# Performance work log

Measured on AMD Instinct MI355X. Metric: run time of the kernel, lower is better.

Reference implementation:

```python
import jax, jax.numpy as jnp
import numpy as np

DIM = 2048
N_HEADS = 32
N_KV_HEADS = 8
HEAD_DIM = 64
REPEATS = N_HEADS // N_KV_HEADS
SCALE = HEAD_DIM ** -0.5
L = 2048
B = 1


def rotary_matrix(context_len, d):
    # Dense (L, d, d) RoPE rotation matrix, exactly as get_rotary_matrix1.
    pos = jnp.arange(1, context_len + 1, dtype=jnp.float32)[:, None]
    i = jnp.arange(d // 2)
    theta = 10000.0 ** (-2.0 * i.astype(jnp.float32) / d)
    m_theta = pos * theta  # (L, d/2)
    cos_v, sin_v = jnp.cos(m_theta), jnp.sin(m_theta)
    R = jnp.zeros((context_len, d, d), dtype=jnp.float32)
    R = R.at[:, 2 * i, 2 * i].set(cos_v)
    R = R.at[:, 2 * i, 2 * i + 1].set(-sin_v)
    R = R.at[:, 2 * i + 1, 2 * i].set(sin_v)
    R = R.at[:, 2 * i + 1, 2 * i + 1].set(cos_v)
    return R


def causal_mask(context_len):
    idx = jnp.arange(context_len)
    return (idx[:, None] < idx[None, :]).astype(jnp.float32) * -1e9


def setup_inputs() -> dict:
    key = jax.random.key(0)
    ks = jax.random.split(key, 5)
    x = jax.random.normal(ks[0], (B, L, DIM), dtype=jnp.float32)
    mask = causal_mask(L)
    wq_w = jax.random.normal(ks[1], (N_HEADS * HEAD_DIM, DIM), dtype=jnp.float32) * 0.02
    wk_w = jax.random.normal(ks[2], (N_KV_HEADS * HEAD_DIM, DIM), dtype=jnp.float32) * 0.02
    wv_w = jax.random.normal(ks[3], (N_KV_HEADS * HEAD_DIM, DIM), dtype=jnp.float32) * 0.02
    wo_w = jax.random.normal(ks[4], (DIM, N_HEADS * HEAD_DIM), dtype=jnp.float32) * 0.02
    return {"x": x, "mask": mask, "wq_w": wq_w, "wk_w": wk_w, "wv_w": wv_w, "wo_w": wo_w}


def reference(x, mask, wq_w, wk_w, wv_w, wo_w):
    Bx, Lx, D = x.shape
    # projections (torch Linear: y = x @ W.T)
    q = jnp.einsum('bld,od->blo', x, wq_w).reshape(Bx, Lx, N_HEADS, HEAD_DIM).transpose(0, 2, 1, 3)
    k = jnp.einsum('bld,od->blo', x, wk_w).reshape(Bx, Lx, N_KV_HEADS, HEAD_DIM).transpose(0, 2, 1, 3)
    v = jnp.einsum('bld,od->blo', x, wv_w).reshape(Bx, Lx, N_KV_HEADS, HEAD_DIM).transpose(0, 2, 1, 3)
    # GQA repeat of kv heads (interleaved, matching concat-unsqueeze-reshape)
    k = jnp.repeat(k, REPEATS, axis=1)
    v = jnp.repeat(v, REPEATS, axis=1)
    # dense-matrix RoPE on q and (repeated) k
    R = rotary_matrix(Lx, HEAD_DIM)
    q = jnp.einsum('bhlj,lij->bhli', q, R)
    k = jnp.einsum('bhlj,lij->bhli', k, R)
    scores = jnp.einsum('bhld,bhmd->bhlm', q, k) * SCALE + mask
    attn = jax.nn.softmax(scores.astype(jnp.float32), axis=-1)
    out = jnp.einsum('bhlm,bhmd->bhld', attn, v)
    out = out.transpose(0, 2, 1, 3).reshape(Bx, Lx, N_HEADS * HEAD_DIM)
    out = jnp.einsum('blo,do->bld', out, wo_w)
    return out, k, v
```

## Files before the change

### kernel.cpp

```cpp
#include <hip/hip_runtime.h>

typedef __bf16 bf16;
typedef __bf16 bf16x8 __attribute__((ext_vector_type(8)));
typedef float floatx4 __attribute__((ext_vector_type(4)));
typedef float floatx16 __attribute__((ext_vector_type(16)));
typedef unsigned int uint;

#define MFMA16(a, b, c) __builtin_amdgcn_mfma_f32_16x16x32_bf16((a), (b), (c), 0, 0, 0)
#define MFMA32(a, b, c) __builtin_amdgcn_mfma_f32_32x32x16_bf16((a), (b), (c), 0, 0, 0)

__device__ __forceinline__ void gl2lds16(const bf16* g, bf16* l) {
  __builtin_amdgcn_global_load_lds(
      (const __attribute__((address_space(1))) void*)g,
      (__attribute__((address_space(3))) void*)l, 16, 0, 0);
}
__device__ __forceinline__ void wait_vm0() { __builtin_amdgcn_s_waitcnt(0x0f70); }

__device__ __forceinline__ float* slot_ptr(int s, float* o0, float* o1) {
  return s < 512 ? o0 + (size_t)s * 8192 : o1 + (size_t)(s - 512) * 8192;
}
__device__ __forceinline__ const float* slot_ptr_c(int s, const float* o0,
                                                   const float* o1) {
  return s < 512 ? o0 + (size_t)s * 8192 : o1 + (size_t)(s - 512) * 8192;
}

__device__ __forceinline__ void cvt8(const float* __restrict__ s,
                                     bf16* __restrict__ d, int i8) {
  const float4 a = ((const float4*)s)[i8 * 2];
  const float4 b = ((const float4*)s)[i8 * 2 + 1];
  bf16x8 o;
  o[0] = (bf16)a.x; o[1] = (bf16)a.y; o[2] = (bf16)a.z; o[3] = (bf16)a.w;
  o[4] = (bf16)b.x; o[5] = (bf16)b.y; o[6] = (bf16)b.z; o[7] = (bf16)b.w;
  *(bf16x8*)(d + i8 * 8) = o;
}

__global__ __launch_bounds__(256) void convert_kernel(
    const float* __restrict__ x, const float* __restrict__ wq,
    const float* __restrict__ wk, const float* __restrict__ wv,
    const float* __restrict__ wo, bf16* __restrict__ xb,
    bf16* __restrict__ wqb, bf16* __restrict__ wkb, bf16* __restrict__ wvb,
    bf16* __restrict__ wob) {
  const int g = blockIdx.x * 256 + threadIdx.x;
  if (g < 524288) cvt8(x, xb, g);
  else if (g < 1048576) cvt8(wq, wqb, g - 524288);
  else if (g < 1179648) cvt8(wk, wkb, g - 1048576);
  else if (g < 1310720) cvt8(wv, wvb, g - 1179648);
  else cvt8(wo, wob, g - 1310720);
}

template <typename OutT>
__device__ __forceinline__ void gemm_tile_body64(
    const bf16* __restrict__ A, int lda,
    const bf16* __restrict__ B, int ldb,
    OutT* __restrict__ C, int ldc, int K,
    bf16* S) {
  const int t = threadIdx.x;
  const int w = t >> 6, lane = t & 63;
  const int l15 = lane & 15, qd = lane >> 4;
  const int wr = w >> 1, wc = w & 1;

  floatx4 acc[2][4];
#pragma unroll
  for (int i = 0; i < 2; ++i)
#pragma unroll
    for (int j = 0; j < 4; ++j) acc[i][j] = (floatx4){0.f, 0.f, 0.f, 0.f};

  const bf16* gb[6];
  int lo[6];
#pragma unroll
  for (int i = 0; i < 6; ++i) {
    const int u = w + 4 * i;
    lo[i] = u * 512 + lane * 8;
    if (u < 8) {
      gb[i] = A + ((u >> 1) * 16 + l15) * lda + (u & 1) * 32 + qd * 8;
    } else {
      const int v = u - 8;
      gb[i] = B + ((v >> 1) * 16 + l15) * ldb + (v & 1) * 32 + qd * 8;
    }
  }

#define STG64(kt_, buf_)                                            \
  {                                                                 \
    bf16* d_ = S + (buf_) * 12288;                                  \
    _Pragma("unroll")                                               \
    for (int i_ = 0; i_ < 6; ++i_)                                  \
      gl2lds16(gb[i_] + (kt_) * 64, d_ + lo[i_]);                   \
  }

  const int NT = K >> 6;
  STG64(0, 0);
  wait_vm0();
  __syncthreads();
  int cur = 0;
  for (int kt = 0; kt < NT; ++kt) {
    if (kt + 1 < NT) STG64(kt + 1, cur ^ 1);
    const bf16* Ab = S + cur * 12288;
    const bf16* Bb = Ab + 4096;
    bf16x8 a[2][2], b[4][2];
#pragma unroll
    for (int i = 0; i < 2; ++i)
#pragma unroll
      for (int kk = 0; kk < 2; ++kk)
        a[i][kk] =
            *(const bf16x8*)(Ab + ((wr * 2 + i) * 2 + kk) * 512 + lane * 8);
#pragma unroll
    for (int j = 0; j < 4; ++j)
#pragma unroll
      for (int kk = 0; kk < 2; ++kk)
        b[j][kk] =
            *(const bf16x8*)(Bb + ((wc * 4 + j) * 2 + kk) * 512 + lane * 8);
#pragma unroll
    for (int kk = 0; kk < 2; ++kk)
#pragma unroll
      for (int i = 0; i < 2; ++i)
#pragma unroll
        for (int j = 0; j < 4; ++j)
          acc[i][j] = MFMA16(a[i][kk], b[j][kk], acc[i][j]);
    wait_vm0();
    __builtin_amdgcn_sched_barrier(0);
    __builtin_amdgcn_s_barrier();
    __builtin_amdgcn_sched_barrier(0);
    cur ^= 1;
  }
#undef STG64

#pragma unroll
  for (int i = 0; i < 2; ++i)
#pragma unroll
    for (int j = 0; j < 4; ++j) {
      const int row = wr * 32 + i * 16 + qd * 4;
      const int col = wc * 64 + j * 16 + l15;
#pragma unroll
      for (int r = 0; r < 4; ++r)
        C[(row + r) * ldc + col] = (OutT)acc[i][j][r];
    }
}

__global__ __launch_bounds__(256) void gemm_qkv(
    const bf16* __restrict__ x, const bf16* __restrict__ wq,
    const bf16* __restrict__ wk, const bf16* __restrict__ wv,
    bf16* __restrict__ Qws, bf16* __restrict__ Kh, bf16* __restrict__ Vh,
    bf16* __restrict__ Vt) {
  __shared__ bf16 SM[17152];
  bf16* As = SM;
  bf16* Bs = SM + 4096;
  const int bid = blockIdx.y * 24 + blockIdx.x;
  const int swz = (bid & 7) * 48 + (bid >> 3);
  const int nb = swz % 24;
  const int m0 = (swz / 24) * 128;
  const bf16* B;
  if (nb < 16) B = wq + nb * 128 * 2048;
  else if (nb < 20) B = wk + (nb - 16) * 128 * 2048;
  else B = wv + (nb - 20) * 128 * 2048;

  const int t = threadIdx.x;
  const int w = t >> 6, lane = t & 63;
  const int l15 = lane & 15, qd = lane >> 4;
  const int wr = w >> 1, wc = w & 1;

  floatx4 acc[4][4];
#pragma unroll
  for (int i = 0; i < 4; ++i)
#pragma unroll
    for (int j = 0; j < 4; ++j) acc[i][j] = (floatx4){0.f, 0.f, 0.f, 0.f};

  const bf16* A = x + m0 * 2048;
  const int mt0 = w, mt1 = w + 4;
  const int kseg = qd * 8;
  const bf16* ga0 = A + (mt0 * 16 + l15) * 2048 + kseg;
  const bf16* ga1 = A + (mt1 * 16 + l15) * 2048 + kseg;
  const bf16* gb0 = B + (mt0 * 16 + l15) * 2048 + kseg;
  const bf16* gb1 = B + (mt1 * 16 + l15) * 2048 + kseg;
  bf16* lA0 = As + mt0 * 512 + lane * 8;
  bf16* lA1 = As + mt1 * 512 + lane * 8;
  bf16* lB0 = Bs + mt0 * 512 + lane * 8;
  bf16* lB1 = Bs + mt1 * 512 + lane * 8;

  for (int k0 = 0; k0 < 2048; k0 += 32) {
    gl2lds16(ga0 + k0, lA0);
    gl2lds16(ga1 + k0, lA1);
    gl2lds16(gb0 + k0, lB0);
    gl2lds16(gb1 + k0, lB1);
    wait_vm0();
    __syncthreads();

    bf16x8 a[4], b[4];
#pragma unroll
    for (int i = 0; i < 4; ++i)
      a[i] = *(const bf16x8*)(As + (wr * 4 + i) * 512 + lane * 8);
#pragma unroll
    for (int j = 0; j < 4; ++j)
      b[j] = *(const bf16x8*)(Bs + (wc * 4 + j) * 512 + lane * 8);
#pragma unroll
    for (int i = 0; i < 4; ++i)
#pragma unroll
      for (int j = 0; j < 4; ++j) acc[i][j] = MFMA16(a[i], b[j], acc[i][j]);
    __syncthreads();
  }

#pragma unroll
  for (int i = 0; i < 4; ++i)
#pragma unroll
    for (int j = 0; j < 4; ++j) {
      const int row = wr * 64 + i * 16 + qd * 4;
      const int col = wc * 64 + j * 16 + l15;
#pragma unroll
      for (int r = 0; r < 4; ++r)
        SM[(row + r) * 134 + col] = (bf16)acc[i][j][r];
    }
  __syncthreads();

  const float NEG_LOG2_10000_D32 = -0.4152410118609203f;
  if (nb < 16) {
#pragma unroll
    for (int k = 0; k < 8; ++k) {
      const int u = t + (k << 8);
      const int row = u >> 4, c8 = (u & 15) << 3;
      const bf16x8 v = *(const bf16x8*)&SM[row * 134 + c8];
      const float base = (float)(m0 + row + 1);
      bf16x8 ov;
#pragma unroll
      for (int p = 0; p < 4; ++p) {
        const int a = ((c8 & 63) >> 1) + p;
        float s, c;
        __sincosf(base * exp2f(NEG_LOG2_10000_D32 * (float)a), &s, &c);
        const float x0 = (float)v[2 * p], x1 = (float)v[2 * p + 1];
        ov[2 * p] = (bf16)(c * x0 - s * x1);
        ov[2 * p + 1] = (bf16)(s * x0 + c * x1);
      }
      *(bf16x8*)&Qws[(m0 + row) * 2048 + nb * 128 + c8] = ov;
    }
  } else if (nb < 20) {
#pragma unroll
    for (int k = 0; k < 8; ++k) {
      const int u = t + (k << 8);
      const int row = u >> 4, c8 = (u & 15) << 3;
      const bf16x8 v = *(const bf16x8*)&SM[row * 134 + c8];
      const float base = (float)(m0 + row + 1);
      bf16x8 ov;
#pragma unroll
      for (int p = 0; p < 4; ++p) {
        const int a = ((c8 & 63) >> 1) + p;
        float s, c;
        __sincosf(base * exp2f(NEG_LOG2_10000_D32 * (float)a), &s, &c);
        const float x0 = (float)v[2 * p], x1 = (float)v[2 * p + 1];
        ov[2 * p] = (bf16)(c * x0 - s * x1);
        ov[2 * p + 1] = (bf16)(s * x0 + c * x1);
      }
      const int g512 = (nb - 16) * 128 + c8;
      const int kvh = g512 >> 6, d8 = g512 & 63;
      *(bf16x8*)&Kh[(kvh * 2048 + m0 + row) * 64 + d8] = ov;
    }
  } else {
#pragma unroll
    for (int k = 0; k < 8; ++k) {
      const int u = t + (k << 8);
      const int row = u >> 4, c8 = (u & 15) << 3;
      const bf16x8 v = *(const bf16x8*)&SM[row * 134 + c8];
      const int g512 = (nb - 20) * 128 + c8;
      const int kvh = g512 >> 6, d8 = g512 & 63;
      *(bf16x8*)&Vh[(kvh * 2048 + m0 + row) * 64 + d8] = v;
    }
#pragma unroll
    for (int k = 0; k < 8; ++k) {
      const int u = t + (k << 8);
      const int col = u >> 4, r8 = (u & 15) << 3;
      bf16x8 v;
#pragma unroll
      for (int jj = 0; jj < 8; ++jj) v[jj] = SM[(r8 + jj) * 134 + col];
      const int g512 = (nb - 20) * 128 + col;
      const int kvh = g512 >> 6, d = g512 & 63;
      *(bf16x8*)&Vt[kvh * 131072 + d * 2048 + m0 + r8] = v;
    }
  }
}

__global__ __launch_bounds__(256) void gemm_o(
    const bf16* __restrict__ Ows, const bf16* __restrict__ wo,
    float* __restrict__ out, const bf16* __restrict__ Kh,
    const bf16* __restrict__ Vh, float* __restrict__ kout,
    float* __restrict__ vout) {
  __shared__ bf16 S[24576];
  const int bid = blockIdx.y * 16 + blockIdx.x;
  const int swz = (bid & 7) * 64 + (bid >> 3);
  const int n0 = (swz & 15) * 128;
  const int m0 = (swz >> 4) * 64;
  gemm_tile_body64<float>(Ows + m0 * 2048, 2048, wo + n0 * 2048, 2048,
                          out + m0 * 2048 + n0, 2048, 2048, S);

  const int g = bid * 256 + (int)threadIdx.x;
  for (uint u = (uint)g; u < 262144u; u += 131072u) {
    const uint u2 = u & 131071u;
    const bf16* src = (u < 131072u) ? Kh : Vh;
    float* dst = (u < 131072u) ? kout : vout;
    const int kvh2 = u2 >> 14;
    const int rr = u2 & 16383;
    const int l = rr >> 3, d8 = (rr & 7) * 8;
    const bf16x8 v = *(const bf16x8*)(src + (kvh2 * 2048 + l) * 64 + d8);
    float4 f0, f1;
    f0.x = (float)v[0]; f0.y = (float)v[1]; f0.z = (float)v[2]; f0.w = (float)v[3];
    f1.x = (float)v[4]; f1.y = (float)v[5]; f1.z = (float)v[6]; f1.w = (float)v[7];
#pragma unroll
    for (int rep = 0; rep < 4; ++rep) {
      float* o2 = dst + (((kvh2 * 4 + rep) * 2048 + l) * 64 + d8);
      *(float4*)o2 = f0;
      *(float4*)(o2 + 4) = f1;
    }
  }
}

__global__ __launch_bounds__(256) void flash_kernel(
    const bf16* __restrict__ Qws, const bf16* __restrict__ Kh,
    const bf16* __restrict__ Vt, bf16* __restrict__ Ows,
    float* __restrict__ Op0, float* __restrict__ Op1, float* __restrict__ ML) {
  __shared__ bf16 SMEM[16384];

  const int h = blockIdx.y;
  const int bx = blockIdx.x;
  int qt, seg, kts, kte, slot;
  if (bx < 4) {
    qt = bx; seg = -1; kts = 0; kte = 2 * qt + 2; slot = -1;
  } else if (bx < 12) {
    const int j = bx - 4;
    qt = 4 + (j >> 1); seg = j & 1;
    const int nkt = 2 * qt + 2;
    kts = seg * nkt / 2; kte = (seg + 1) * nkt / 2;
    slot = h * 32 + (bx - 4);
  } else {
    const int j = bx - 12;
    qt = 8 + j / 3; seg = j % 3;
    const int nkt = 2 * qt + 2;
    kts = seg * nkt / 3; kte = (seg + 1) * nkt / 3;
    slot = h * 32 + (bx - 4);
  }
  const int kh = h >> 2;
  const int q0 = qt * 128;
  const int t = threadIdx.x, w = t >> 6, lane = t & 63;
  const int l31 = lane & 31, hf = lane >> 5;
  const int qw = q0 + w * 32;

  const int s0 = w, s1 = w + 4;
  const bf16* gK0 = Kh + kh * 131072 + ((s0 >> 2) * 32 + l31) * 64 + (s0 & 3) * 16 + hf * 8;
  const bf16* gK1 = Kh + kh * 131072 + ((s1 >> 2) * 32 + l31) * 64 + (s1 & 3) * 16 + hf * 8;
  const bf16* gV0 = Vt + kh * 131072 + ((s0 >> 2) * 32 + l31) * 2048 + (s0 & 3) * 16 + hf * 8;
  const bf16* gV1 = Vt + kh * 131072 + ((s1 >> 2) * 32 + l31) * 2048 + (s1 & 3) * 16 + hf * 8;

  {
    const int nb = kts & 1;
    gl2lds16(gK0 + kts * 4096, &SMEM[nb * 8192 + s0 * 512 + lane * 8]);
    gl2lds16(gK1 + kts * 4096, &SMEM[nb * 8192 + s1 * 512 + lane * 8]);
    gl2lds16(gV0 + kts * 64, &SMEM[nb * 8192 + 4096 + s0 * 512 + lane * 8]);
    gl2lds16(gV1 + kts * 64, &SMEM[nb * 8192 + 4096 + s1 * 512 + lane * 8]);
  }

  bf16x8 qf[4];
  {
    const bf16* qrow = Qws + (qw + l31) * 2048 + h * 64 + hf * 8;
#pragma unroll
    for (int c = 0; c < 4; ++c) qf[c] = *(const bf16x8*)(qrow + c * 16);
  }

  floatx16 o[2] = {};
  float mrun = -3e38f, lrun = 0.f;

  const float C = 0.1803368801f;
  for (int kt = kts; kt < kte; ++kt) {
    wait_vm0();
    __syncthreads();
    if (kt + 1 < kte) {
      const int nb = (kt + 1) & 1;
      const int koff = (kt + 1) * 4096, voff = (kt + 1) * 64;
      gl2lds16(gK0 + koff, &SMEM[nb * 8192 + s0 * 512 + lane * 8]);
      gl2lds16(gK1 + koff, &SMEM[nb * 8192 + s1 * 512 + lane * 8]);
      gl2lds16(gV0 + voff, &SMEM[nb * 8192 + 4096 + s0 * 512 + lane * 8]);
      gl2lds16(gV1 + voff, &SMEM[nb * 8192 + 4096 + s1 * 512 + lane * 8]);
    }
    const int kt64 = kt * 64;
    if (kt64 > qw + 31) continue;
    const bf16* Kb = &SMEM[(kt & 1) * 8192];
    const bf16* Vb = Kb + 4096;

    floatx16 st[2];
    __builtin_amdgcn_s_setprio(1);
#pragma unroll
    for (int tt = 0; tt < 2; ++tt) {
      floatx16 z = {};
#pragma unroll
      for (int c = 0; c < 4; ++c) {
        const bf16x8 kf = *(const bf16x8*)(Kb + (tt * 4 + c) * 512 + lane * 8);
        z = MFMA32(kf, qf[c], z);
      }
      st[tt] = z;
    }
    __builtin_amdgcn_s_setprio(0);
    if (kt64 + 64 > qw) {
      const int myq = qw + l31;
#pragma unroll
      for (int tt = 0; tt < 2; ++tt)
#pragma unroll
        for (int r = 0; r < 16; ++r) {
          const int key = kt64 + tt * 32 + (r & 3) + 8 * (r >> 2) + 4 * hf;
          if (key > myq) st[tt][r] = -1e30f;
        }
    }
    float ma = -3e38f, mb = -3e38f, mc = -3e38f, md = -3e38f;
#pragma unroll
    for (int tt = 0; tt < 2; ++tt)
#pragma unroll
      for (int r = 0; r < 16; r += 4) {
        ma = fmaxf(ma, st[tt][r + 0]);
        mb = fmaxf(mb, st[tt][r + 1]);
        mc = fmaxf(mc, st[tt][r + 2]);
        md = fmaxf(md, st[tt][r + 3]);
      }
    float mx = fmaxf(fmaxf(ma, mb), fmaxf(mc, md));
    mx = fmaxf(mx, __shfl_xor(mx, 32));
    const bool defer = __all((mx - mrun) * C <= 8.f);
    if (!defer) {
      const float mn = fmaxf(mrun, mx);
      const float al = __builtin_amdgcn_exp2f((mrun - mn) * C);
      lrun *= al;
#pragma unroll
      for (int n = 0; n < 2; ++n)
#pragma unroll
        for (int r = 0; r < 16; ++r) o[n][r] *= al;
      mrun = mn;
    }
    float ra = 0.f, rb = 0.f, rc = 0.f, rd = 0.f;
#pragma unroll
    for (int tt = 0; tt < 2; ++tt)
#pragma unroll
      for (int r = 0; r < 16; r += 4) {
        const float p0 = __builtin_amdgcn_exp2f((st[tt][r + 0] - mrun) * C);
        const float p1 = __builtin_amdgcn_exp2f((st[tt][r + 1] - mrun) * C);
        const float p2 = __builtin_amdgcn_exp2f((st[tt][r + 2] - mrun) * C);
        const float p3 = __builtin_amdgcn_exp2f((st[tt][r + 3] - mrun) * C);
        st[tt][r + 0] = p0; ra += p0;
        st[tt][r + 1] = p1; rb += p1;
        st[tt][r + 2] = p2; rc += p2;
        st[tt][r + 3] = p3; rd += p3;
      }
    float rs = (ra + rb) + (rc + rd);
    rs += __shfl_xor(rs, 32);
    lrun += rs;

    uint pk[2][4][2];
#pragma unroll
    for (int tt = 0; tt < 2; ++tt)
#pragma unroll
      for (int g = 0; g < 4; ++g)
#pragma unroll
        for (int p = 0; p < 2; ++p) {
          union { bf16 h2[2]; uint u; } cv;
          cv.h2[0] = (bf16)st[tt][4 * g + 2 * p];
          cv.h2[1] = (bf16)st[tt][4 * g + 2 * p + 1];
          pk[tt][g][p] = cv.u;
        }
    uint own_[2][2][2], rv[2][2][2];
#pragma unroll
    for (int tt = 0; tt < 2; ++tt)
#pragma unroll
      for (int gam = 0; gam < 2; ++gam)
#pragma unroll
        for (int p = 0; p < 2; ++p) {
          own_[tt][gam][p] = hf ? pk[tt][2 * gam + 1][p] : pk[tt][2 * gam][p];
          const uint snd = hf ? pk[tt][2 * gam][p] : pk[tt][2 * gam + 1][p];
          rv[tt][gam][p] = (uint)__shfl_xor((int)snd, 32);
        }
    __builtin_amdgcn_s_setprio(1);
#pragma unroll
    for (int c = 0; c < 4; ++c) {
      const int tt = c >> 1, gam = c & 1;
      union { uint u[4]; bf16x8 v; } pf;
      pf.u[0] = hf ? rv[tt][gam][0] : own_[tt][gam][0];
      pf.u[1] = hf ? rv[tt][gam][1] : own_[tt][gam][1];
      pf.u[2] = hf ? own_[tt][gam][0] : rv[tt][gam][0];
      pf.u[3] = hf ? own_[tt][gam][1] : rv[tt][gam][1];
#pragma unroll
      for (int n = 0; n < 2; ++n)
        o[n] = MFMA32(*(const bf16x8*)(Vb + (n * 4 + c) * 512 + lane * 8),
                      pf.v, o[n]);
    }
    __builtin_amdgcn_s_setprio(0);
  }

  if (seg < 0) {
    __syncthreads();
    bf16* Osh = SMEM;
    const float inv = 1.f / lrun;
#pragma unroll
    for (int n = 0; n < 2; ++n)
#pragma unroll
      for (int r = 0; r < 16; ++r) {
        const int dl = n * 32 + (r & 3) + 8 * (r >> 2) + 4 * hf;
        Osh[(w * 32 + l31) * 66 + dl] = (bf16)(o[n][r] * inv);
      }
    __syncthreads();
#pragma unroll
    for (int i = 0; i < 4; ++i) {
      const int row = (t >> 3) + i * 32;
      const int col = (t & 7) * 8;
      const bf16x8 vv = *(const bf16x8*)&Osh[row * 66 + col];
      *(bf16x8*)&Ows[(q0 + row) * 2048 + h * 64 + col] = vv;
    }
  } else {
    float* Op = slot_ptr(slot, Op0, Op1);
#pragma unroll
    for (int n = 0; n < 2; ++n)
#pragma unroll
      for (int r = 0; r < 16; ++r) {
        const int dl = n * 32 + (r & 3) + 8 * (r >> 2) + 4 * hf;
        Op[dl * 128 + w * 32 + l31] = o[n][r];
      }
    if (hf == 0) {
      ML[slot * 256 + w * 32 + l31] = mrun;
      ML[slot * 256 + 128 + w * 32 + l31] = lrun;
    }
  }
}

__global__ __launch_bounds__(256) void combine_kernel(
    const float* __restrict__ Op0, const float* __restrict__ Op1,
    const float* __restrict__ ML, bf16* __restrict__ Ows) {
  __shared__ bf16 Osh[128 * 66];
  const int b = blockIdx.x;
  const int h = b / 12, qi = b % 12;
  const int qt = 4 + qi;
  const int q0 = qt * 128;
  const bool three = (qi >= 4);
  const int slot0 = h * 32 + (three ? 8 + (qi - 4) * 3 : qi * 2);
  const int t = threadIdx.x;
  const int row = t & 127, dh = t >> 7;
  const float C = 0.1803368801f;
  const float m0 = ML[(slot0 + 0) * 256 + row], l0 = ML[(slot0 + 0) * 256 + 128 + row];
  const float m1 = ML[(slot0 + 1) * 256 + row], l1 = ML[(slot0 + 1) * 256 + 128 + row];
  const float m2 = three ? ML[(slot0 + 2) * 256 + row] : -3e38f;
  const float l2 = three ? ML[(slot0 + 2) * 256 + 128 + row] : 0.f;
  const float m = fmaxf(fmaxf(m0, m1), m2);
  const float w0 = __builtin_amdgcn_exp2f((m0 - m) * C);
  const float w1 = __builtin_amdgcn_exp2f((m1 - m) * C);
  const float w2 = three ? __builtin_amdgcn_exp2f((m2 - m) * C) : 0.f;
  const float inv = 1.f / (l0 * w0 + l1 * w1 + l2 * w2);
  const float* P0 = slot_ptr_c(slot0 + 0, Op0, Op1);
  const float* P1 = slot_ptr_c(slot0 + 1, Op0, Op1);
  const float* P2 = three ? slot_ptr_c(slot0 + 2, Op0, Op1) : P0;
#pragma unroll
  for (int j = 0; j < 32; ++j) {
    const int d = dh * 32 + j;
    const float v = (P0[d * 128 + row] * w0 + P1[d * 128 + row] * w1 +
                     P2[d * 128 + row] * w2) *
                    inv;
    Osh[row * 66 + d] = (bf16)v;
  }
  __syncthreads();
#pragma unroll
  for (int i = 0; i < 4; ++i) {
    const int r2 = (t >> 3) + i * 32;
    const int col = (t & 7) * 8;
    const bf16x8 vv = *(const bf16x8*)&Osh[r2 * 66 + col];
    *(bf16x8*)&Ows[(q0 + r2) * 2048 + h * 64 + col] = vv;
  }
}

extern "C" void kernel_launch(void* const* d_in, const int* in_sizes, int n_in,
                              void* d_out, int out_size, void* d_ws,
                              size_t ws_size, hipStream_t stream) {
  const float* x = (const float*)d_in[0];
  const float* wq = (const float*)d_in[2];
  const float* wk = (const float*)d_in[3];
  const float* wv = (const float*)d_in[4];
  const float* wo = (const float*)d_in[5];

  float* out = (float*)d_out;
  float* kout = out + 4194304;
  float* vout = out + 8388608;

  bf16* ws = (bf16*)d_ws;
  bf16* xb = ws;
  bf16* wqb = xb + 4194304;
  bf16* wkb = wqb + 4194304;
  bf16* wvb = wkb + 1048576;
  bf16* wob = wvb + 1048576;
  bf16* Qws = wob + 4194304;
  bf16* Kws = Qws + 4194304;
  bf16* Vh = Kws + 1048576;
  bf16* Vt = Vh + 1048576;
  bf16* Ows = Vt + 1048576;
  bf16* Kh = Ows + 4194304;
  float* Op0 = out;
  float* Op1 = (float*)ws;
  float* MLf = (float*)Kws;

  convert_kernel<<<dim3(7168), dim3(256), 0, stream>>>(x, wq, wk, wv, wo, xb,
                                                       wqb, wkb, wvb, wob);
  gemm_qkv<<<dim3(24, 16), dim3(256), 0, stream>>>(xb, wqb, wkb, wvb, Qws, Kh,
                                                   Vh, Vt);
  flash_kernel<<<dim3(36, 32), dim3(256), 0, stream>>>(Qws, Kh, Vt, Ows, Op0,
                                                       Op1, MLf);
  combine_kernel<<<dim3(384), dim3(256), 0, stream>>>(Op0, Op1, MLf, Ows);
  gemm_o<<<dim3(16, 32), dim3(256), 0, stream>>>(Ows, wob, out, Kh, Vh, kout,
                                                 vout);
}
```

Baseline: 282.1 us.

## Deepen QKV GEMM K-step, reverse flash block order, fold wo conversion into flash

The QKV GEMM now stages a 64-wide K slice per iteration instead of 32. This halves the number of barrier and wait round-trips, at the cost of more LDS per block. The flash kernel walks its query tiles in reverse so the longest causal tiles start first, which should improve tail balance. The fp32-to-bf16 conversion of wo moves out of the upfront convert kernel into a grid-strided epilogue of the flash kernel, overlapping it with attention's uneven tail. That epilogue adds memory traffic to the flash blocks.

```diff
diff --git a/kernel.cpp b/kernel.cpp
--- a/kernel.cpp
+++ b/kernel.cpp
@@ -37,15 +37,13 @@
 __global__ __launch_bounds__(256) void convert_kernel(
     const float* __restrict__ x, const float* __restrict__ wq,
     const float* __restrict__ wk, const float* __restrict__ wv,
-    const float* __restrict__ wo, bf16* __restrict__ xb,
-    bf16* __restrict__ wqb, bf16* __restrict__ wkb, bf16* __restrict__ wvb,
-    bf16* __restrict__ wob) {
+    bf16* __restrict__ xb, bf16* __restrict__ wqb, bf16* __restrict__ wkb,
+    bf16* __restrict__ wvb) {
   const int g = blockIdx.x * 256 + threadIdx.x;
   if (g < 524288) cvt8(x, xb, g);
   else if (g < 1048576) cvt8(wq, wqb, g - 524288);
   else if (g < 1179648) cvt8(wk, wkb, g - 1048576);
-  else if (g < 1310720) cvt8(wv, wvb, g - 1179648);
-  else cvt8(wo, wob, g - 1310720);
+  else cvt8(wv, wvb, g - 1179648);
 }
 
 template <typename OutT>
@@ -143,7 +141,7 @@
     bf16* __restrict__ Vt) {
   __shared__ bf16 SM[17152];
   bf16* As = SM;
-  bf16* Bs = SM + 4096;
+  bf16* Bs = SM + 8192;
   const int bid = blockIdx.y * 24 + blockIdx.x;
   const int swz = (bid & 7) * 48 + (bid >> 3);
   const int nb = swz % 24;
@@ -171,30 +169,47 @@
   const bf16* ga1 = A + (mt1 * 16 + l15) * 2048 + kseg;
   const bf16* gb0 = B + (mt0 * 16 + l15) * 2048 + kseg;
   const bf16* gb1 = B + (mt1 * 16 + l15) * 2048 + kseg;
-  bf16* lA0 = As + mt0 * 512 + lane * 8;
-  bf16* lA1 = As + mt1 * 512 + lane * 8;
-  bf16* lB0 = Bs + mt0 * 512 + lane * 8;
-  bf16* lB1 = Bs + mt1 * 512 + lane * 8;
-
-  for (int k0 = 0; k0 < 2048; k0 += 32) {
-    gl2lds16(ga0 + k0, lA0);
-    gl2lds16(ga1 + k0, lA1);
-    gl2lds16(gb0 + k0, lB0);
-    gl2lds16(gb1 + k0, lB1);
+  bf16* lA00 = As + (mt0 * 2 + 0) * 512 + lane * 8;
+  bf16* lA01 = As + (mt0 * 2 + 1) * 512 + lane * 8;
+  bf16* lA10 = As + (mt1 * 2 + 0) * 512 + lane * 8;
+  bf16* lA11 = As + (mt1 * 2 + 1) * 512 + lane * 8;
+  bf16* lB00 = Bs + (mt0 * 2 + 0) * 512 + lane * 8;
+  bf16* lB01 = Bs + (mt0 * 2 + 1) * 512 + lane * 8;
+  bf16* lB10 = Bs + (mt1 * 2 + 0) * 512 + lane * 8;
+  bf16* lB11 = Bs + (mt1 * 2 + 1) * 512 + lane * 8;
+
+  for (int k0 = 0; k0 < 2048; k0 += 64) {
+    gl2lds16(ga0 + k0, lA00);
+    gl2lds16(ga0 + k0 + 32, lA01);
+    gl2lds16(ga1 + k0, lA10);
+    gl2lds16(ga1 + k0 + 32, lA11);
+    gl2lds16(gb0 + k0, lB00);
+    gl2lds16(gb0 + k0 + 32, lB01);
+    gl2lds16(gb1 + k0, lB10);
+    gl2lds16(gb1 + k0 + 32, lB11);
     wait_vm0();
     __syncthreads();
 
-    bf16x8 a[4], b[4];
+    bf16x8 a[4][2], b[4][2];
 #pragma unroll
     for (int i = 0; i < 4; ++i)
-      a[i] = *(const bf16x8*)(As + (wr * 4 + i) * 512 + lane * 8);
+#pragma unroll
+      for (int kk = 0; kk < 2; ++kk)
+        a[i][kk] =
+            *(const bf16x8*)(As + ((wr * 4 + i) * 2 + kk) * 512 + lane * 8);
 #pragma unroll
     for (int j = 0; j < 4; ++j)
-      b[j] = *(const bf16x8*)(Bs + (wc * 4 + j) * 512 + lane * 8);
-#pragma unroll
-    for (int i = 0; i < 4; ++i)
-#pragma unroll
-      for (int j = 0; j < 4; ++j) acc[i][j] = MFMA16(a[i], b[j], acc[i][j]);
+#pragma unroll
+      for (int kk = 0; kk < 2; ++kk)
+        b[j][kk] =
+            *(const bf16x8*)(Bs + ((wc * 4 + j) * 2 + kk) * 512 + lane * 8);
+#pragma unroll
+    for (int kk = 0; kk < 2; ++kk)
+#pragma unroll
+      for (int i = 0; i < 4; ++i)
+#pragma unroll
+        for (int j = 0; j < 4; ++j)
+          acc[i][j] = MFMA16(a[i][kk], b[j][kk], acc[i][j]);
     __syncthreads();
   }
 
@@ -312,11 +327,12 @@
 __global__ __launch_bounds__(256) void flash_kernel(
     const bf16* __restrict__ Qws, const bf16* __restrict__ Kh,
     const bf16* __restrict__ Vt, bf16* __restrict__ Ows,
-    float* __restrict__ Op0, float* __restrict__ Op1, float* __restrict__ ML) {
+    float* __restrict__ Op0, float* __restrict__ Op1, float* __restrict__ ML,
+    const float* __restrict__ wo, bf16* __restrict__ wob) {
   __shared__ bf16 SMEM[16384];
 
   const int h = blockIdx.y;
-  const int bx = blockIdx.x;
+  const int bx = 35 - (int)blockIdx.x;
   int qt, seg, kts, kte, slot;
   if (bx < 4) {
     qt = bx; seg = -1; kts = 0; kte = 2 * qt + 2; slot = -1;
@@ -516,6 +532,12 @@
       ML[slot * 256 + w * 32 + l31] = mrun;
       ML[slot * 256 + 128 + w * 32 + l31] = lrun;
     }
+  }
+
+  {
+    const int bidf = (int)blockIdx.y * 36 + (int)blockIdx.x;
+    for (uint u = (uint)(bidf * 256 + t); u < 524288u; u += 294912u)
+      cvt8(wo, wob, (int)u);
   }
 }
 
@@ -591,12 +613,12 @@
   float* Op1 = (float*)ws;
   float* MLf = (float*)Kws;
 
-  convert_kernel<<<dim3(7168), dim3(256), 0, stream>>>(x, wq, wk, wv, wo, xb,
-                                                       wqb, wkb, wvb, wob);
+  convert_kernel<<<dim3(5120), dim3(256), 0, stream>>>(x, wq, wk, wv, xb, wqb,
+                                                       wkb, wvb);
   gemm_qkv<<<dim3(24, 16), dim3(256), 0, stream>>>(xb, wqb, wkb, wvb, Qws, Kh,
                                                    Vh, Vt);
   flash_kernel<<<dim3(36, 32), dim3(256), 0, stream>>>(Qws, Kh, Vt, Ows, Op0,
-                                                       Op1, MLf);
+                                                       Op1, MLf, wo, wob);
   combine_kernel<<<dim3(384), dim3(256), 0, stream>>>(Op0, Op1, MLf, Ows);
   gemm_o<<<dim3(16, 32), dim3(256), 0, stream>>>(Ows, wob, out, Kh, Vh, kout,
                                                  vout);
```

Result: no change. 277.9 us (median of 2 runs) (-1.5%).
